# Performance work log

Measured on AMD Instinct MI355X. Metric: run time of the kernel, lower is better.

## Reference

```python
import jax, jax.numpy as jnp
import numpy as np

NENTITY = 100000
NRELATION = 500
HIDDEN = 256
GAMMA = 12.0
BATCH = 8


def setup_inputs() -> dict:
    key = jax.random.key(0)
    k1, k2, k3, k4 = jax.random.split(key, 4)
    entity_embedding = jax.random.normal(k1, (NENTITY, HIDDEN), dtype=jnp.float32)
    relation_embedding = jax.random.normal(k2, (NRELATION, HIDDEN), dtype=jnp.float32)
    positive_sample = jax.random.randint(k3, (BATCH, 3), 0, NRELATION, dtype=jnp.int64)
    negative_sample = jax.random.randint(k4, (BATCH, NENTITY), 0, NENTITY, dtype=jnp.int64)
    return {
        "entity_embedding": entity_embedding,
        "relation_embedding": relation_embedding,
        "positive_sample": positive_sample,
        "negative_sample": negative_sample,
    }


def reference(entity_embedding, relation_embedding, positive_sample, negative_sample):
    # 'tail-batch' mode of KGEModel.forward + TransE scoring.
    # head, relation come from the positive triple; tail is every negative candidate.
    head = entity_embedding[positive_sample[:, 0]][:, None, :]      # [B, 1, H]
    relation = relation_embedding[positive_sample[:, 1]][:, None, :]  # [B, 1, H]
    tail = entity_embedding[negative_sample]                          # [B, N, H]
    # score = gamma - || head + relation - tail ||_1
    score = GAMMA - jnp.sum(jnp.abs(head + relation - tail), axis=-1)  # [B, N]
    return score
```

## Files before the change

### kernel.cpp

```cpp
#include <hip/hip_runtime.h>

#define HIDDEN 256
#define GAMMA_F 12.0f
#define BATCH 8

__global__ __launch_bounds__(256) void kge_dist_kernel(
    const float* __restrict__ ent,
    const float* __restrict__ rel,
    const int*  __restrict__ pos,
    float* __restrict__ dist,
    int ngroups, int nent)
{
    const int lane = threadIdx.x & 63;
    const int wave_gid = (blockIdx.x * 256 + threadIdx.x) >> 6;
    const int nwaves = gridDim.x * 4;

    float4 hr[BATCH];
    #pragma unroll
    for (int b = 0; b < BATCH; ++b) {
        const int hidx = pos[b * 3 + 0];
        const int ridx = pos[b * 3 + 1];
        const float4 h4 = *(const float4*)(ent + (size_t)hidx * HIDDEN + lane * 4);
        const float4 r4 = *(const float4*)(rel + (size_t)ridx * HIDDEN + lane * 4);
        hr[b] = make_float4(h4.x + r4.x, h4.y + r4.y, h4.z + r4.z, h4.w + r4.w);
    }

    for (int grp = wave_gid; grp < ngroups; grp += nwaves) {
        const float* base = ent + (size_t)grp * 8 * HIDDEN + lane * 4;

        float4 t[8];
        #pragma unroll
        for (int r = 0; r < 8; ++r)
            t[r] = *(const float4*)(base + r * HIDDEN);

        float res = 0.0f;
        #pragma unroll
        for (int r = 0; r < 8; ++r) {
            float acc[BATCH];
            #pragma unroll
            for (int b = 0; b < BATCH; ++b) {
                acc[b] = fabsf(hr[b].x - t[r].x) + fabsf(hr[b].y - t[r].y)
                       + fabsf(hr[b].z - t[r].z) + fabsf(hr[b].w - t[r].w);
            }
            float v[4];
            {
                const bool p = lane & 1;
                #pragma unroll
                for (int k = 0; k < 4; ++k) {
                    const float keep = p ? acc[2 * k + 1] : acc[2 * k];
                    const float give = p ? acc[2 * k]     : acc[2 * k + 1];
                    v[k] = keep + __shfl_xor(give, 1, 64);
                }
            }
            float w2[2];
            {
                const bool p = (lane >> 1) & 1;
                #pragma unroll
                for (int k = 0; k < 2; ++k) {
                    const float keep = p ? v[2 * k + 1] : v[2 * k];
                    const float give = p ? v[2 * k]     : v[2 * k + 1];
                    w2[k] = keep + __shfl_xor(give, 2, 64);
                }
            }
            float s;
            {
                const bool p = (lane >> 2) & 1;
                const float keep = p ? w2[1] : w2[0];
                const float give = p ? w2[0] : w2[1];
                s = keep + __shfl_xor(give, 4, 64);
            }
            s += __shfl_xor(s, 8, 64);
            s += __shfl_xor(s, 16, 64);
            s += __shfl_xor(s, 32, 64);
            if ((lane >> 3) == r) res = GAMMA_F - s;
        }
        dist[(size_t)grp * 64 + lane] = res;
    }

    if (wave_gid == 0) {
        for (int e = ngroups * 8; e < nent; ++e) {
            const float4 t4 = *(const float4*)(ent + (size_t)e * HIDDEN + lane * 4);
            float acc[BATCH];
            #pragma unroll
            for (int b = 0; b < BATCH; ++b) {
                acc[b] = fabsf(hr[b].x - t4.x) + fabsf(hr[b].y - t4.y)
                       + fabsf(hr[b].z - t4.z) + fabsf(hr[b].w - t4.w);
            }
            float v[4];
            {
                const bool p = lane & 1;
                #pragma unroll
                for (int k = 0; k < 4; ++k) {
                    const float keep = p ? acc[2 * k + 1] : acc[2 * k];
                    const float give = p ? acc[2 * k]     : acc[2 * k + 1];
                    v[k] = keep + __shfl_xor(give, 1, 64);
                }
            }
            float w2[2];
            {
                const bool p = (lane >> 1) & 1;
                #pragma unroll
                for (int k = 0; k < 2; ++k) {
                    const float keep = p ? v[2 * k + 1] : v[2 * k];
                    const float give = p ? v[2 * k]     : v[2 * k + 1];
                    w2[k] = keep + __shfl_xor(give, 2, 64);
                }
            }
            float s;
            {
                const bool p = (lane >> 2) & 1;
                const float keep = p ? w2[1] : w2[0];
                const float give = p ? w2[0] : w2[1];
                s = keep + __shfl_xor(give, 4, 64);
            }
            s += __shfl_xor(s, 8, 64);
            s += __shfl_xor(s, 16, 64);
            s += __shfl_xor(s, 32, 64);
            if (lane < BATCH) dist[(size_t)e * BATCH + lane] = GAMMA_F - s;
        }
    }
}

__global__ __launch_bounds__(256) void kge_gather_kernel(
    const int*  __restrict__ neg,
    const float* __restrict__ dist,
    float* __restrict__ out,
    int nneg)
{
    const int b = blockIdx.y;
    const int n = (blockIdx.x * 256 + threadIdx.x) * 2;
    if (n + 1 < nneg) {
        const int2 idx = *(const int2*)(neg + (size_t)b * nneg + n);
        float2 r;
        r.x = dist[(size_t)idx.x * BATCH + b];
        r.y = dist[(size_t)idx.y * BATCH + b];
        *(float2*)(out + (size_t)b * nneg + n) = r;
    } else if (n < nneg) {
        out[(size_t)b * nneg + n] =
            dist[(size_t)neg[(size_t)b * nneg + n] * BATCH + b];
    }
}

extern "C" void kernel_launch(void* const* d_in, const int* in_sizes, int n_in,
                              void* d_out, int out_size, void* d_ws, size_t ws_size,
                              hipStream_t stream) {
    const float* ent = (const float*)d_in[0];
    const float* rel = (const float*)d_in[1];
    const int*   pos = (const int*)d_in[2];
    const int*   neg = (const int*)d_in[3];
    float* out = (float*)d_out;

    const int nent = in_sizes[0] / HIDDEN;
    const int nneg = in_sizes[3] / BATCH;
    float* dist = (float*)d_ws;

    const int ngroups = nent / 8;
    kge_dist_kernel<<<1024, 256, 0, stream>>>(ent, rel, pos, dist, ngroups, nent);

    const int npairs = (nneg + 1) / 2;
    dim3 gridB((npairs + 255) / 256, BATCH);
    kge_gather_kernel<<<gridB, 256, 0, stream>>>(neg, dist, out, nneg);
}
```

Baseline: 166.2 us.

## Process one entity per wave iteration and raise occupancy with more blocks

The distance kernel now handles one entity row per wave iteration instead of loading eight rows at once, which removes the eight-row register tile and the separate serial tail loop. The launch bound asks for 8 blocks per CU and the grid grows to 2048 blocks, trading per-wave memory-level parallelism for more resident waves. Each iteration now stores only 8 floats from 8 lanes instead of a full 64-lane coalesced store, so write efficiency may drop.

```diff
diff --git a/kernel.cpp b/kernel.cpp
--- a/kernel.cpp
+++ b/kernel.cpp
@@ -4,16 +4,15 @@
 #define GAMMA_F 12.0f
 #define BATCH 8
 
-__global__ __launch_bounds__(256) void kge_dist_kernel(
+__global__ __launch_bounds__(256, 8) void kge_dist_kernel(
     const float* __restrict__ ent,
     const float* __restrict__ rel,
     const int*  __restrict__ pos,
     float* __restrict__ dist,
-    int ngroups, int nent)
+    int nent, int nwaves)
 {
     const int lane = threadIdx.x & 63;
     const int wave_gid = (blockIdx.x * 256 + threadIdx.x) >> 6;
-    const int nwaves = gridDim.x * 4;
 
     float4 hr[BATCH];
     #pragma unroll
@@ -25,99 +24,49 @@
         hr[b] = make_float4(h4.x + r4.x, h4.y + r4.y, h4.z + r4.z, h4.w + r4.w);
     }
 
-    for (int grp = wave_gid; grp < ngroups; grp += nwaves) {
-        const float* base = ent + (size_t)grp * 8 * HIDDEN + lane * 4;
+    for (int e = wave_gid; e < nent; e += nwaves) {
+        const float4 t4 = *(const float4*)(ent + (size_t)e * HIDDEN + lane * 4);
 
-        float4 t[8];
+        float acc[BATCH];
         #pragma unroll
-        for (int r = 0; r < 8; ++r)
-            t[r] = *(const float4*)(base + r * HIDDEN);
+        for (int b = 0; b < BATCH; ++b) {
+            acc[b] = fabsf(hr[b].x - t4.x) + fabsf(hr[b].y - t4.y)
+                   + fabsf(hr[b].z - t4.z) + fabsf(hr[b].w - t4.w);
+        }
 
-        float res = 0.0f;
-        #pragma unroll
-        for (int r = 0; r < 8; ++r) {
-            float acc[BATCH];
+        float v[4];
+        {
+            const bool p = lane & 1;
             #pragma unroll
-            for (int b = 0; b < BATCH; ++b) {
-                acc[b] = fabsf(hr[b].x - t[r].x) + fabsf(hr[b].y - t[r].y)
-                       + fabsf(hr[b].z - t[r].z) + fabsf(hr[b].w - t[r].w);
+            for (int k = 0; k < 4; ++k) {
+                const float keep = p ? acc[2 * k + 1] : acc[2 * k];
+                const float give = p ? acc[2 * k]     : acc[2 * k + 1];
+                v[k] = keep + __shfl_xor(give, 1, 64);
             }
-            float v[4];
-            {
-                const bool p = lane & 1;
-                #pragma unroll
-                for (int k = 0; k < 4; ++k) {
-                    const float keep = p ? acc[2 * k + 1] : acc[2 * k];
-                    const float give = p ? acc[2 * k]     : acc[2 * k + 1];
-                    v[k] = keep + __shfl_xor(give, 1, 64);
-                }
+        }
+        float w2[2];
+        {
+            const bool p = (lane >> 1) & 1;
+            #pragma unroll
+            for (int k = 0; k < 2; ++k) {
+                const float keep = p ? v[2 * k + 1] : v[2 * k];
+                const float give = p ? v[2 * k]     : v[2 * k + 1];
+                w2[k] = keep + __shfl_xor(give, 2, 64);
             }
-            float w2[2];
-            {
-                const bool p = (lane >> 1) & 1;
-                #pragma unroll
-                for (int k = 0; k < 2; ++k) {
-                    const float keep = p ? v[2 * k + 1] : v[2 * k];
-                    const float give = p ? v[2 * k]     : v[2 * k + 1];
-                    w2[k] = keep + __shfl_xor(give, 2, 64);
-                }
-            }
-            float s;
-            {
-                const bool p = (lane >> 2) & 1;
-                const float keep = p ? w2[1] : w2[0];
-                const float give = p ? w2[0] : w2[1];
-                s = keep + __shfl_xor(give, 4, 64);
-            }
-            s += __shfl_xor(s, 8, 64);
-            s += __shfl_xor(s, 16, 64);
-            s += __shfl_xor(s, 32, 64);
-            if ((lane >> 3) == r) res = GAMMA_F - s;
         }
-        dist[(size_t)grp * 64 + lane] = res;
-    }
+        float s;
+        {
+            const bool p = (lane >> 2) & 1;
+            const float keep = p ? w2[1] : w2[0];
+            const float give = p ? w2[0] : w2[1];
+            s = keep + __shfl_xor(give, 4, 64);
+        }
+        s += __shfl_xor(s, 8, 64);
+        s += __shfl_xor(s, 16, 64);
+        s += __shfl_xor(s, 32, 64);
 
-    if (wave_gid == 0) {
-        for (int e = ngroups * 8; e < nent; ++e) {
-            const float4 t4 = *(const float4*)(ent + (size_t)e * HIDDEN + lane * 4);
-            float acc[BATCH];
-            #pragma unroll
-            for (int b = 0; b < BATCH; ++b) {
-                acc[b] = fabsf(hr[b].x - t4.x) + fabsf(hr[b].y - t4.y)
-                       + fabsf(hr[b].z - t4.z) + fabsf(hr[b].w - t4.w);
-            }
-            float v[4];
-            {
-                const bool p = lane & 1;
-                #pragma unroll
-                for (int k = 0; k < 4; ++k) {
-                    const float keep = p ? acc[2 * k + 1] : acc[2 * k];
-                    const float give = p ? acc[2 * k]     : acc[2 * k + 1];
-                    v[k] = keep + __shfl_xor(give, 1, 64);
-                }
-            }
-            float w2[2];
-            {
-                const bool p = (lane >> 1) & 1;
-                #pragma unroll
-                for (int k = 0; k < 2; ++k) {
-                    const float keep = p ? v[2 * k + 1] : v[2 * k];
-                    const float give = p ? v[2 * k]     : v[2 * k + 1];
-                    w2[k] = keep + __shfl_xor(give, 2, 64);
-                }
-            }
-            float s;
-            {
-                const bool p = (lane >> 2) & 1;
-                const float keep = p ? w2[1] : w2[0];
-                const float give = p ? w2[0] : w2[1];
-                s = keep + __shfl_xor(give, 4, 64);
-            }
-            s += __shfl_xor(s, 8, 64);
-            s += __shfl_xor(s, 16, 64);
-            s += __shfl_xor(s, 32, 64);
-            if (lane < BATCH) dist[(size_t)e * BATCH + lane] = GAMMA_F - s;
-        }
+        if (lane < BATCH)
+            dist[(size_t)e * BATCH + lane] = GAMMA_F - s;
     }
 }
 
@@ -154,8 +103,10 @@
     const int nneg = in_sizes[3] / BATCH;
     float* dist = (float*)d_ws;
 
-    const int ngroups = nent / 8;
-    kge_dist_kernel<<<1024, 256, 0, stream>>>(ent, rel, pos, dist, ngroups, nent);
+    const int nblocks = 2048;
+    const int nwaves = nblocks * 4;
+    kge_dist_kernel<<<nblocks, 256, 0, stream>>>(ent, rel, pos, dist,
+                                                 nent, nwaves);
 
     const int npairs = (nneg + 1) / 2;
     dim3 gridB((npairs + 255) / 256, BATCH);
```

Result: no change. 163.9 us, median of 2 (-1.4%).

## Store distance table batch-major and widen gather to four elements per thread

Applied to the files above, without the earlier changes.

Changes the intermediate distance table from entity-major [nent][8] to batch-major [8][nent]. A ds_bpermute transpose inside each wave makes the stores land in the new layout, so each batch's gather reads one contiguous plane with better cache locality. The change also loads tail rows one at a time instead of prefetching all eight, which lowers register pressure, and adds a launch_bounds occupancy hint and a doubled grid size. Loading rows on demand may expose more memory latency, and the strided stores now write 8-element segments spread across eight planes.

```diff
diff --git a/kernel.cpp b/kernel.cpp
--- a/kernel.cpp
+++ b/kernel.cpp
@@ -4,16 +4,15 @@
 #define GAMMA_F 12.0f
 #define BATCH 8
 
-__global__ __launch_bounds__(256) void kge_dist_kernel(
+__global__ __launch_bounds__(256, 8) void kge_dist_kernel(
     const float* __restrict__ ent,
     const float* __restrict__ rel,
     const int*  __restrict__ pos,
     float* __restrict__ dist,
-    int ngroups, int nent)
+    int ngroups, int nent, int nwaves)
 {
     const int lane = threadIdx.x & 63;
     const int wave_gid = (blockIdx.x * 256 + threadIdx.x) >> 6;
-    const int nwaves = gridDim.x * 4;
 
     float4 hr[BATCH];
     #pragma unroll
@@ -26,21 +25,19 @@
     }
 
     for (int grp = wave_gid; grp < ngroups; grp += nwaves) {
-        const float* base = ent + (size_t)grp * 8 * HIDDEN + lane * 4;
+        const int e0 = grp * 8;
+        float res = 0.0f;
 
-        float4 t[8];
-        #pragma unroll
-        for (int r = 0; r < 8; ++r)
-            t[r] = *(const float4*)(base + r * HIDDEN);
-
-        float res = 0.0f;
         #pragma unroll
         for (int r = 0; r < 8; ++r) {
+            const float4 t4 =
+                *(const float4*)(ent + (size_t)(e0 + r) * HIDDEN + lane * 4);
+
             float acc[BATCH];
             #pragma unroll
             for (int b = 0; b < BATCH; ++b) {
-                acc[b] = fabsf(hr[b].x - t[r].x) + fabsf(hr[b].y - t[r].y)
-                       + fabsf(hr[b].z - t[r].z) + fabsf(hr[b].w - t[r].w);
+                acc[b] = fabsf(hr[b].x - t4.x) + fabsf(hr[b].y - t4.y)
+                       + fabsf(hr[b].z - t4.z) + fabsf(hr[b].w - t4.w);
             }
             float v[4];
             {
@@ -74,7 +71,11 @@
             s += __shfl_xor(s, 32, 64);
             if ((lane >> 3) == r) res = GAMMA_F - s;
         }
-        dist[(size_t)grp * 64 + lane] = res;
+
+        const int src = ((lane & 7) * 8 + (lane >> 3)) * 4;
+        const float val =
+            __int_as_float(__builtin_amdgcn_ds_bpermute(src, __float_as_int(res)));
+        dist[(size_t)(lane >> 3) * nent + e0 + (lane & 7)] = val;
     }
 
     if (wave_gid == 0) {
@@ -116,7 +117,7 @@
             s += __shfl_xor(s, 8, 64);
             s += __shfl_xor(s, 16, 64);
             s += __shfl_xor(s, 32, 64);
-            if (lane < BATCH) dist[(size_t)e * BATCH + lane] = GAMMA_F - s;
+            if (lane < BATCH) dist[(size_t)lane * nent + e] = GAMMA_F - s;
         }
     }
 }
@@ -125,19 +126,22 @@
     const int*  __restrict__ neg,
     const float* __restrict__ dist,
     float* __restrict__ out,
-    int nneg)
+    int nneg, int nent)
 {
     const int b = blockIdx.y;
-    const int n = (blockIdx.x * 256 + threadIdx.x) * 2;
-    if (n + 1 < nneg) {
-        const int2 idx = *(const int2*)(neg + (size_t)b * nneg + n);
-        float2 r;
-        r.x = dist[(size_t)idx.x * BATCH + b];
-        r.y = dist[(size_t)idx.y * BATCH + b];
-        *(float2*)(out + (size_t)b * nneg + n) = r;
-    } else if (n < nneg) {
-        out[(size_t)b * nneg + n] =
-            dist[(size_t)neg[(size_t)b * nneg + n] * BATCH + b];
+    const float* plane = dist + (size_t)b * nent;
+    const int n = (blockIdx.x * 256 + threadIdx.x) * 4;
+    if (n + 3 < nneg) {
+        const int4 idx = *(const int4*)(neg + (size_t)b * nneg + n);
+        float4 r;
+        r.x = plane[idx.x];
+        r.y = plane[idx.y];
+        r.z = plane[idx.z];
+        r.w = plane[idx.w];
+        *(float4*)(out + (size_t)b * nneg + n) = r;
+    } else {
+        for (int i = n; i < nneg; ++i)
+            out[(size_t)b * nneg + i] = plane[neg[(size_t)b * nneg + i]];
     }
 }
 
@@ -155,9 +159,12 @@
     float* dist = (float*)d_ws;
 
     const int ngroups = nent / 8;
-    kge_dist_kernel<<<1024, 256, 0, stream>>>(ent, rel, pos, dist, ngroups, nent);
+    const int nblocks = 2048;
+    const int nwaves = nblocks * 4;
+    kge_dist_kernel<<<nblocks, 256, 0, stream>>>(ent, rel, pos, dist,
+                                                 ngroups, nent, nwaves);
 
-    const int npairs = (nneg + 1) / 2;
-    dim3 gridB((npairs + 255) / 256, BATCH);
-    kge_gather_kernel<<<gridB, 256, 0, stream>>>(neg, dist, out, nneg);
+    const int nquads = (nneg + 3) / 4;
+    dim3 gridB((nquads + 255) / 256, BATCH);
+    kge_gather_kernel<<<gridB, 256, 0, stream>>>(neg, dist, out, nneg, nent);
 }
```

After: 169.3 us. About the same (+1.8%).
